# Performance work log

Measured on AMD Instinct MI355X. Metric: run time of the kernel, lower is better.

The kernel has to match this reference:

```python
import jax, jax.numpy as jnp
import numpy as np

N_NODES = 4096
N_EDGES = 65536
BS = 16
LEAKY_SLOPE = 0.01
BN_EPS = 1e-5


def _init(key, shape, scale=0.02):
    return (jax.random.normal(key, shape, dtype=jnp.float32) * scale)


def setup_inputs() -> dict:
    key = jax.random.key(0)
    ks = jax.random.split(key, 20)
    x_in = jax.random.normal(ks[0], (N_NODES, 8500), dtype=jnp.float32)
    edge_index = jax.random.randint(ks[1], (2, N_EDGES), 0, N_NODES, dtype=jnp.int64)
    return {
        "x_in": x_in,
        "edge_index": edge_index,
        # SAGEConv params: Wl (neighbor lin, with bias), Wr (root lin, no bias)
        "W1l": _init(ks[2], (320, 8500)), "b1": jnp.zeros((320,), jnp.float32), "W1r": _init(ks[3], (320, 8500)),
        "W2l": _init(ks[4], (180, 320)),  "b2": jnp.zeros((180,), jnp.float32), "W2r": _init(ks[5], (180, 320)),
        "W3l": _init(ks[6], (90, 180)),   "b3": jnp.zeros((90,), jnp.float32),  "W3r": _init(ks[7], (90, 180)),
        "W4l": _init(ks[8], (50, 90)),    "b4": jnp.zeros((50,), jnp.float32),  "W4r": _init(ks[9], (50, 90)),
        "Wf1": _init(ks[10], (32, 50)),   "bf1": jnp.zeros((32,), jnp.float32),
        "Wf2": _init(ks[11], (16, 32)),   "bf2": jnp.zeros((16,), jnp.float32),
        "Wf3": _init(ks[12], (1, 16)),    "bf3": jnp.zeros((1,), jnp.float32),
    }


def _sage(x, src, dst, Wl, bl, Wr):
    # PyG SAGEConv: out = lin_l(mean_{j in N(i)} x_j) + lin_r(x_i)
    agg = jax.ops.segment_sum(x[src], dst, num_segments=N_NODES)          # [N, F]
    deg = jax.ops.segment_sum(jnp.ones_like(dst, dtype=x.dtype), dst, num_segments=N_NODES)
    mean = agg / jnp.maximum(deg, 1.0)[:, None]
    return mean @ Wl.T + bl + x @ Wr.T


def _leaky(x):
    return jnp.where(x >= 0, x, LEAKY_SLOPE * x)


def _bn(x):
    # F.batch_norm(x, None, None, training=True): per-feature, biased var, no affine
    m = jnp.mean(x, axis=0)
    v = jnp.mean((x - m) ** 2, axis=0)
    return (x - m) / jnp.sqrt(v + BN_EPS)


def reference(x_in, edge_index,
              W1l, b1, W1r, W2l, b2, W2r, W3l, b3, W3r, W4l, b4, W4r,
              Wf1, bf1, Wf2, bf2, Wf3, bf3):
    src, dst = edge_index[0], edge_index[1]
    x = _bn(_leaky(_sage(x_in, src, dst, W1l, b1, W1r)))
    x = _bn(_leaky(_sage(x, src, dst, W2l, b2, W2r)))
    x = _bn(_leaky(_sage(x, src, dst, W3l, b3, W3r)))
    x = _bn(_leaky(_sage(x, src, dst, W4l, b4, W4r)))
    # get_batch: label i -> floor(i / (N/BS)); global_add_pool == segment sum
    x = x.reshape(BS, N_NODES // BS, -1).sum(axis=1)                      # [BS, 50]
    x = x @ Wf1.T + bf1
    x = x @ Wf2.T + bf2
    x = x @ Wf3.T + bf3
    return x
```

## Files before the change

### kernel.cpp

```cpp
#include <hip/hip_runtime.h>
#include <stdint.h>

#define NN 4096
#define NE 65536
#define LEAKY 0.01f
#define BN_EPS 1e-5f

typedef float f32x4 __attribute__((ext_vector_type(4)));
typedef __bf16 bf16x8 __attribute__((ext_vector_type(8)));

static __device__ __forceinline__ unsigned short f2bf(float v) {
  unsigned int u = __float_as_uint(v);
  u += 0x7fff + ((u >> 16) & 1);
  return (unsigned short)(u >> 16);
}

typedef __attribute__((address_space(1))) void gvoid;
typedef __attribute__((address_space(3))) void lvoid;

static __device__ __forceinline__ void async16(const void* g, void* l) {
  __builtin_amdgcn_global_load_lds((gvoid*)(uintptr_t)g,
                                   (lvoid*)(uint32_t)(uintptr_t)l, 16, 0, 0);
}


__global__ void pack_x1(const float* __restrict__ x, unsigned short* __restrict__ out) {
  int idx = blockIdx.x * 256 + threadIdx.x;
  int row = idx / 8512;
  int k = idx - row * 8512;
  float v = (k < 8500) ? x[(size_t)row * 8500 + k] : 0.f;
  out[idx] = f2bf(v);
}

__global__ void pack_w(const float* __restrict__ Wl, const float* __restrict__ Wr,
                       unsigned short* __restrict__ dst, int Fout, int Fin, int Kp, int total) {
  int idx = blockIdx.x * 256 + threadIdx.x;
  if (idx >= total) return;
  int row = idx / Kp;
  int k = idx - row * Kp;
  float v = 0.f;
  if (k < Fin) {
    if (row < Fout)            v = Wl[(size_t)row * Fin + k];
    else if (row < 2 * Fout)   v = Wr[(size_t)(row - Fout) * Fin + k];
  }
  dst[idx] = f2bf(v);
}


__global__ void count_deg(const int* __restrict__ dst_idx, int* __restrict__ deg) {
  int e = blockIdx.x * 256 + threadIdx.x;
  if (e < NE) atomicAdd(&deg[dst_idx[e]], 1);
}

__global__ __launch_bounds__(1024) void scan_deg(const int* __restrict__ deg,
                                                 int* __restrict__ off) {
  __shared__ int s[NN];
  int t = threadIdx.x;
  for (int i = t; i < NN; i += 1024) s[i] = deg[i];
  __syncthreads();
  for (int step = 1; step < NN; step <<= 1) {
    int v[4];
#pragma unroll
    for (int j = 0; j < 4; ++j) {
      int i = t + j * 1024;
      v[j] = (i >= step) ? s[i - step] : 0;
    }
    __syncthreads();
#pragma unroll
    for (int j = 0; j < 4; ++j) s[t + j * 1024] += v[j];
    __syncthreads();
  }
  for (int i = t; i < NN; i += 1024) off[i] = (i == 0) ? 0 : s[i - 1];
}

__global__ void scatter_edges(const int* __restrict__ src_idx,
                              const int* __restrict__ dst_idx,
                              const int* __restrict__ off, int* __restrict__ cursor,
                              int* __restrict__ eix) {
  int e = blockIdx.x * 256 + threadIdx.x;
  if (e < NE) {
    int d = dst_idx[e];
    int pos = atomicAdd(&cursor[d], 1);
    eix[off[d] + pos] = src_idx[e];
  }
}

__global__ __launch_bounds__(256) void gemm_bt(const unsigned short* __restrict__ A,
                                               const unsigned short* __restrict__ B,
                                               float* __restrict__ C, int N, int K) {
  __shared__ unsigned short smem[2 * 128 * 64];
  unsigned short* As = smem;
  unsigned short* Bs = smem + 128 * 64;

  const int t = threadIdx.x;
  const int bm = blockIdx.x, bn = blockIdx.y;
  const int lane = t & 63;
  const int wave = t >> 6;
  const int wm = (wave & 1) * 64, wn = (wave >> 1) * 64;
  const int l16 = lane & 15, quad = lane >> 4;

  const int ksteps = K >> 6;
  const int gz = (int)gridDim.z;
  const int per = (ksteps + gz - 1) / gz;
  const int k0 = (int)blockIdx.z * per;
  int k1 = k0 + per; if (k1 > ksteps) k1 = ksteps;

  f32x4 zero = {0.f, 0.f, 0.f, 0.f};
  f32x4 acc[4][4];
#pragma unroll
  for (int i = 0; i < 4; ++i)
#pragma unroll
    for (int j = 0; j < 4; ++j) acc[i][j] = zero;

  const int srow = t >> 3;
  const int scol = (t & 7) * 8;
  const unsigned short* Abase = A + (size_t)(bm * 128) * K + scol;
  const unsigned short* Bbase = B + (size_t)(bn * 128) * K + scol;

  for (int kt = k0; kt < k1; ++kt) {
    const unsigned short* Ag = Abase + kt * 64;
    const unsigned short* Bg = Bbase + kt * 64;
#pragma unroll
    for (int p = 0; p < 4; ++p) {
      int row = p * 32 + srow;
      async16(Ag + (size_t)row * K, &As[row * 64 + scol]);
    }
#pragma unroll
    for (int p = 0; p < 4; ++p) {
      int row = p * 32 + srow;
      async16(Bg + (size_t)row * K, &Bs[row * 64 + scol]);
    }
    __syncthreads();
#pragma unroll
    for (int kh = 0; kh < 2; ++kh) {
      bf16x8 af[4], bfr[4];
#pragma unroll
      for (int i = 0; i < 4; ++i)
        af[i] = *(const bf16x8*)&As[(wm + i * 16 + l16) * 64 + kh * 32 + quad * 8];
#pragma unroll
      for (int j = 0; j < 4; ++j)
        bfr[j] = *(const bf16x8*)&Bs[(wn + j * 16 + l16) * 64 + kh * 32 + quad * 8];
#pragma unroll
      for (int i = 0; i < 4; ++i)
#pragma unroll
        for (int j = 0; j < 4; ++j)
          acc[i][j] = __builtin_amdgcn_mfma_f32_16x16x32_bf16(af[i], bfr[j], acc[i][j], 0, 0, 0);
    }
    __syncthreads();
  }

  const bool use_atomic = (gridDim.z > 1);
#pragma unroll
  for (int i = 0; i < 4; ++i) {
    int rbase = bm * 128 + wm + i * 16 + quad * 4;
#pragma unroll
    for (int j = 0; j < 4; ++j) {
      int col = bn * 128 + wn + j * 16 + l16;
      float* cp = C + (size_t)rbase * N + col;
#pragma unroll
      for (int r = 0; r < 4; ++r) {
        if (use_atomic) atomicAdd(cp + (size_t)r * N, acc[i][j][r]);
        else            cp[(size_t)r * N] = acc[i][j][r];
      }
    }
  }
}

__global__ void sage_agg(const float* __restrict__ y, const int* __restrict__ off,
                         const int* __restrict__ deg, const int* __restrict__ eix,
                         const float* __restrict__ bias, float* __restrict__ z,
                         int F, int ldy) {
  int i = blockIdx.x;
  int f = blockIdx.y * 64 + threadIdx.x;
  if (f >= F) return;
  int start = off[i], d = deg[i];
  float s = 0.f;
  for (int e = 0; e < d; ++e) {
    int src = eix[start + e];
    s += y[(size_t)src * ldy + f];
  }
  int dm = d > 1 ? d : 1;
  float v = s / (float)dm + y[(size_t)i * ldy + F + f] + bias[f];
  z[(size_t)i * F + f] = (v >= 0.f) ? v : LEAKY * v;
}


__global__ void bn_stats(const float* __restrict__ z, float* __restrict__ mrs, int F) {
  int f = blockIdx.x;
  int t = threadIdx.x;
  float s = 0.f, s2 = 0.f;
  for (int i = t; i < NN; i += 256) {
    float v = z[(size_t)i * F + f];
    s += v; s2 += v * v;
  }
  __shared__ float rs[256], rs2[256];
  rs[t] = s; rs2[t] = s2;
  __syncthreads();
  for (int o = 128; o > 0; o >>= 1) {
    if (t < o) { rs[t] += rs[t + o]; rs2[t] += rs2[t + o]; }
    __syncthreads();
  }
  if (t == 0) {
    float m = rs[0] * (1.f / NN);
    float var = rs2[0] * (1.f / NN) - m * m;
    mrs[f] = m;
    mrs[F + f] = 1.f / sqrtf(var + BN_EPS);
  }
}

__global__ void bn_norm_bf16(const float* __restrict__ z, const float* __restrict__ mrs,
                             unsigned short* __restrict__ xout, int F, int Kp, int total) {
  int idx = blockIdx.x * 256 + threadIdx.x;
  if (idx >= total) return;
  int row = idx / Kp;
  int k = idx - row * Kp;
  float v = 0.f;
  if (k < F) v = (z[(size_t)row * F + k] - mrs[k]) * mrs[F + k];
  xout[idx] = f2bf(v);
}

__global__ void bn_norm_f32(const float* __restrict__ z, const float* __restrict__ mrs,
                            float* __restrict__ xout, int F, int total) {
  int idx = blockIdx.x * 256 + threadIdx.x;
  if (idx >= total) return;
  int row = idx / F;
  int k = idx - row * F;
  xout[idx] = (z[(size_t)row * F + k] - mrs[k]) * mrs[F + k];
}

__global__ void pool_fc(const float* __restrict__ x,
                        const float* __restrict__ Wf1, const float* __restrict__ bf1,
                        const float* __restrict__ Wf2, const float* __restrict__ bf2,
                        const float* __restrict__ Wf3, const float* __restrict__ bf3,
                        float* __restrict__ out) {
  __shared__ float pool[50];
  __shared__ float h1[32], h2[16];
  int b = blockIdx.x, t = threadIdx.x;
  if (t < 50) {
    float s = 0.f;
    for (int r = 0; r < 256; ++r) s += x[(size_t)(b * 256 + r) * 50 + t];
    pool[t] = s;
  }
  __syncthreads();
  if (t < 32) {
    float s = bf1[t];
    for (int f = 0; f < 50; ++f) s += pool[f] * Wf1[t * 50 + f];
    h1[t] = s;
  }
  __syncthreads();
  if (t < 16) {
    float s = bf2[t];
    for (int f = 0; f < 32; ++f) s += h1[f] * Wf2[t * 32 + f];
    h2[t] = s;
  }
  __syncthreads();
  if (t == 0) {
    float s = bf3[0];
    for (int f = 0; f < 16; ++f) s += h2[f] * Wf3[f];
    out[b] = s;
  }
}


extern "C" void kernel_launch(void* const* d_in, const int* in_sizes, int n_in,
                              void* d_out, int out_size, void* d_ws, size_t ws_size,
                              hipStream_t stream) {
  const float* x_in = (const float*)d_in[0];
  const int* ei = (const int*)d_in[1];
  const float* W1l = (const float*)d_in[2];
  const float* b1  = (const float*)d_in[3];
  const float* W1r = (const float*)d_in[4];
  const float* W2l = (const float*)d_in[5];
  const float* b2  = (const float*)d_in[6];
  const float* W2r = (const float*)d_in[7];
  const float* W3l = (const float*)d_in[8];
  const float* b3  = (const float*)d_in[9];
  const float* W3r = (const float*)d_in[10];
  const float* W4l = (const float*)d_in[11];
  const float* b4  = (const float*)d_in[12];
  const float* W4r = (const float*)d_in[13];
  const float* Wf1 = (const float*)d_in[14];
  const float* bf1 = (const float*)d_in[15];
  const float* Wf2 = (const float*)d_in[16];
  const float* bf2 = (const float*)d_in[17];
  const float* Wf3 = (const float*)d_in[18];
  const float* bf3 = (const float*)d_in[19];
  float* out = (float*)d_out;
  (void)in_sizes; (void)n_in; (void)out_size;

  char* ws = (char*)d_ws;
  size_t off = 0;
  auto alloc = [&](size_t bytes) -> void* {
    void* p = ws + off;
    off = (off + bytes + 255) & ~(size_t)255;
    return p;
  };
  unsigned short* xbf = (unsigned short*)alloc((size_t)NN * 8512 * 2);
  unsigned short* wb1 = (unsigned short*)alloc((size_t)640 * 8512 * 2);
  unsigned short* wb2 = (unsigned short*)alloc((size_t)384 * 320 * 2);
  unsigned short* wb3 = (unsigned short*)alloc((size_t)256 * 192 * 2);
  unsigned short* wb4 = (unsigned short*)alloc((size_t)128 * 128 * 2);
  float* y    = (float*)alloc((size_t)NN * 640 * 4);
  float* z    = (float*)alloc((size_t)NN * 320 * 4);
  float* z4   = (float*)alloc((size_t)NN * 50 * 4);
  float* mrs  = (float*)alloc(2 * 320 * 4);
  int* deg    = (int*)alloc(NN * 4);
  int* cursor = (int*)alloc(NN * 4);
  int* offb   = (int*)alloc(NN * 4);
  int* eix    = (int*)alloc(NE * 4);
  if (ws_size < off) return;

  hipMemsetAsync(deg, 0, 2 * NN * 4, stream);
  hipMemsetAsync(y, 0, (size_t)NN * 640 * 4, stream);

  pack_x1<<<dim3((NN * 8512) / 256), dim3(256), 0, stream>>>(x_in, xbf);
  pack_w<<<dim3((640 * 8512) / 256), dim3(256), 0, stream>>>(W1l, W1r, wb1, 320, 8500, 8512, 640 * 8512);
  pack_w<<<dim3((384 * 320 + 255) / 256), dim3(256), 0, stream>>>(W2l, W2r, wb2, 180, 320, 320, 384 * 320);
  pack_w<<<dim3((256 * 192 + 255) / 256), dim3(256), 0, stream>>>(W3l, W3r, wb3, 90, 180, 192, 256 * 192);
  pack_w<<<dim3((128 * 128 + 255) / 256), dim3(256), 0, stream>>>(W4l, W4r, wb4, 50, 90, 128, 128 * 128);
  count_deg<<<dim3(NE / 256), dim3(256), 0, stream>>>(ei + NE, deg);
  scan_deg<<<dim3(1), dim3(1024), 0, stream>>>(deg, offb);
  scatter_edges<<<dim3(NE / 256), dim3(256), 0, stream>>>(ei, ei + NE, offb, cursor, eix);

  gemm_bt<<<dim3(32, 5, 4), dim3(256), 0, stream>>>(xbf, wb1, y, 640, 8512);
  sage_agg<<<dim3(NN, 5), dim3(64), 0, stream>>>(y, offb, deg, eix, b1, z, 320, 640);
  bn_stats<<<dim3(320), dim3(256), 0, stream>>>(z, mrs, 320);
  bn_norm_bf16<<<dim3((NN * 320) / 256), dim3(256), 0, stream>>>(z, mrs, xbf, 320, 320, NN * 320);

  gemm_bt<<<dim3(32, 3, 1), dim3(256), 0, stream>>>(xbf, wb2, y, 384, 320);
  sage_agg<<<dim3(NN, 3), dim3(64), 0, stream>>>(y, offb, deg, eix, b2, z, 180, 384);
  bn_stats<<<dim3(180), dim3(256), 0, stream>>>(z, mrs, 180);
  bn_norm_bf16<<<dim3((NN * 192) / 256), dim3(256), 0, stream>>>(z, mrs, xbf, 180, 192, NN * 192);

  gemm_bt<<<dim3(32, 2, 1), dim3(256), 0, stream>>>(xbf, wb3, y, 256, 192);
  sage_agg<<<dim3(NN, 2), dim3(64), 0, stream>>>(y, offb, deg, eix, b3, z, 90, 256);
  bn_stats<<<dim3(90), dim3(256), 0, stream>>>(z, mrs, 90);
  bn_norm_bf16<<<dim3((NN * 128) / 256), dim3(256), 0, stream>>>(z, mrs, xbf, 90, 128, NN * 128);

  gemm_bt<<<dim3(32, 1, 1), dim3(256), 0, stream>>>(xbf, wb4, y, 128, 128);
  sage_agg<<<dim3(NN, 1), dim3(64), 0, stream>>>(y, offb, deg, eix, b4, z, 50, 128);
  bn_stats<<<dim3(50), dim3(256), 0, stream>>>(z, mrs, 50);
  bn_norm_f32<<<dim3((NN * 50) / 256), dim3(256), 0, stream>>>(z, mrs, z4, 50, NN * 50);

  pool_fc<<<dim3(16), dim3(64), 0, stream>>>(z4, Wf1, bf1, Wf2, bf2, Wf3, bf3, out);
}
```

Measured before the change: 569.4 us.

## Fuse setup kernels, swizzle LDS layout, split BN stats, fold last BN into pooling

Merges the x/weight bf16 packing and degree counting into one vectorized setup kernel that writes 8-element chunks in a row-rotated swizzled order. The GEMM reads LDS with the matching swizzle to cut bank conflicts. BN statistics become a parallel partial-sum kernel with atomics, and normalization is fused into a vectorized bf16 writer. The last BN is folded algebraically into the pooling kernel, and the layer-1 GEMM split-K rises from 4 to 8. The atomic float sums make results order-dependent, and the single-pass variance can lose precision.

```diff
diff --git a/kernel.cpp b/kernel.cpp
--- a/kernel.cpp
+++ b/kernel.cpp
@@ -8,6 +8,7 @@
 
 typedef float f32x4 __attribute__((ext_vector_type(4)));
 typedef __bf16 bf16x8 __attribute__((ext_vector_type(8)));
+typedef unsigned short u16x8 __attribute__((ext_vector_type(8)));
 
 static __device__ __forceinline__ unsigned short f2bf(float v) {
   unsigned int u = __float_as_uint(v);
@@ -24,33 +25,84 @@
 }
 
 
-__global__ void pack_x1(const float* __restrict__ x, unsigned short* __restrict__ out) {
-  int idx = blockIdx.x * 256 + threadIdx.x;
-  int row = idx / 8512;
-  int k = idx - row * 8512;
-  float v = (k < 8500) ? x[(size_t)row * 8500 + k] : 0.f;
-  out[idx] = f2bf(v);
-}
-
-__global__ void pack_w(const float* __restrict__ Wl, const float* __restrict__ Wr,
-                       unsigned short* __restrict__ dst, int Fout, int Fin, int Kp, int total) {
-  int idx = blockIdx.x * 256 + threadIdx.x;
-  if (idx >= total) return;
-  int row = idx / Kp;
-  int k = idx - row * Kp;
-  float v = 0.f;
-  if (k < Fin) {
-    if (row < Fout)            v = Wl[(size_t)row * Fin + k];
-    else if (row < 2 * Fout)   v = Wr[(size_t)(row - Fout) * Fin + k];
-  }
-  dst[idx] = f2bf(v);
-}
-
-
-__global__ void count_deg(const int* __restrict__ dst_idx, int* __restrict__ deg) {
-  int e = blockIdx.x * 256 + threadIdx.x;
-  if (e < NE) atomicAdd(&deg[dst_idx[e]], 1);
-}
+static __device__ __forceinline__ void pack_w_seg(int lblk, const float* __restrict__ Wl,
+                                                  const float* __restrict__ Wr,
+                                                  unsigned short* __restrict__ dst,
+                                                  int Fout, int Fin, int Kp, int Np) {
+  int nb = Kp >> 3;
+  int idx = lblk * 256 + threadIdx.x;
+  if (idx >= Np * nb) return;
+  int row = idx / nb, kb = idx - row * nb;
+  int g = kb >> 3, b = kb & 7;
+  int dkb = (g << 3) | ((b + row) & 7);
+  const float* src = nullptr;
+  if (row < Fout)          src = Wl + (size_t)row * Fin;
+  else if (row < 2 * Fout) src = Wr + (size_t)(row - Fout) * Fin;
+  u16x8 st;
+#pragma unroll
+  for (int o = 0; o < 8; ++o) {
+    int k = kb * 8 + o;
+    float v = (src && k < Fin) ? src[k] : 0.f;
+    st[o] = f2bf(v);
+  }
+  *(u16x8*)&dst[(size_t)row * Kp + dkb * 8] = st;
+}
+
+#define PX_BLK   17024
+#define PW1_BLK   2660
+#define PW2_BLK     60
+#define PW3_BLK     24
+#define PW4_BLK      8
+#define CD_BLK     256
+#define SETUP_BLK (PX_BLK + PW1_BLK + PW2_BLK + PW3_BLK + PW4_BLK + CD_BLK)
+
+__global__ __launch_bounds__(256) void setup_all(
+    const float* __restrict__ x, const int* __restrict__ dsti,
+    const float* __restrict__ W1l, const float* __restrict__ W1r,
+    const float* __restrict__ W2l, const float* __restrict__ W2r,
+    const float* __restrict__ W3l, const float* __restrict__ W3r,
+    const float* __restrict__ W4l, const float* __restrict__ W4r,
+    unsigned short* __restrict__ xbf, unsigned short* __restrict__ wb1,
+    unsigned short* __restrict__ wb2, unsigned short* __restrict__ wb3,
+    unsigned short* __restrict__ wb4, int* __restrict__ deg) {
+  int blk = blockIdx.x;
+  if (blk < PX_BLK) {
+    int idx = blk * 256 + threadIdx.x;
+    int row = idx / 1064, kb = idx - row * 1064;
+    int g = kb >> 3, b = kb & 7;
+    int dkb = (g << 3) | ((b + row) & 7);
+    const float* src = x + (size_t)row * 8500 + kb * 8;
+    float v[8];
+    if (kb < 1062) {
+      f32x4 a = *(const f32x4*)src;
+      f32x4 c = *(const f32x4*)(src + 4);
+#pragma unroll
+      for (int o = 0; o < 4; ++o) { v[o] = a[o]; v[o + 4] = c[o]; }
+    } else {
+#pragma unroll
+      for (int o = 0; o < 8; ++o) {
+        int k = kb * 8 + o;
+        v[o] = (k < 8500) ? x[(size_t)row * 8500 + k] : 0.f;
+      }
+    }
+    u16x8 st;
+#pragma unroll
+    for (int o = 0; o < 8; ++o) st[o] = f2bf(v[o]);
+    *(u16x8*)&xbf[(size_t)row * 8512 + dkb * 8] = st;
+  } else if (blk < PX_BLK + PW1_BLK) {
+    pack_w_seg(blk - PX_BLK, W1l, W1r, wb1, 320, 8500, 8512, 640);
+  } else if (blk < PX_BLK + PW1_BLK + PW2_BLK) {
+    pack_w_seg(blk - PX_BLK - PW1_BLK, W2l, W2r, wb2, 180, 320, 320, 384);
+  } else if (blk < PX_BLK + PW1_BLK + PW2_BLK + PW3_BLK) {
+    pack_w_seg(blk - PX_BLK - PW1_BLK - PW2_BLK, W3l, W3r, wb3, 90, 180, 192, 256);
+  } else if (blk < PX_BLK + PW1_BLK + PW2_BLK + PW3_BLK + PW4_BLK) {
+    pack_w_seg(blk - PX_BLK - PW1_BLK - PW2_BLK - PW3_BLK, W4l, W4r, wb4, 50, 90, 128, 128);
+  } else {
+    int e = (blk - (SETUP_BLK - CD_BLK)) * 256 + threadIdx.x;
+    atomicAdd(&deg[dsti[e]], 1);
+  }
+}
+
 
 __global__ __launch_bounds__(1024) void scan_deg(const int* __restrict__ deg,
                                                  int* __restrict__ off) {
@@ -133,13 +185,14 @@
     __syncthreads();
 #pragma unroll
     for (int kh = 0; kh < 2; ++kh) {
+      const int s8 = ((kh * 4 + quad + l16) & 7) * 8;
       bf16x8 af[4], bfr[4];
 #pragma unroll
       for (int i = 0; i < 4; ++i)
-        af[i] = *(const bf16x8*)&As[(wm + i * 16 + l16) * 64 + kh * 32 + quad * 8];
+        af[i] = *(const bf16x8*)&As[(wm + i * 16 + l16) * 64 + s8];
 #pragma unroll
       for (int j = 0; j < 4; ++j)
-        bfr[j] = *(const bf16x8*)&Bs[(wn + j * 16 + l16) * 64 + kh * 32 + quad * 8];
+        bfr[j] = *(const bf16x8*)&Bs[(wn + j * 16 + l16) * 64 + s8];
 #pragma unroll
       for (int i = 0; i < 4; ++i)
 #pragma unroll
@@ -185,50 +238,54 @@
 }
 
 
-__global__ void bn_stats(const float* __restrict__ z, float* __restrict__ mrs, int F) {
-  int f = blockIdx.x;
-  int t = threadIdx.x;
+__global__ __launch_bounds__(256) void bn_part(const float* __restrict__ z,
+                                               float* __restrict__ sums, int F) {
+  int tx = threadIdx.x, ty = threadIdx.y;
+  int f = blockIdx.x * 64 + tx;
   float s = 0.f, s2 = 0.f;
-  for (int i = t; i < NN; i += 256) {
-    float v = z[(size_t)i * F + f];
-    s += v; s2 += v * v;
-  }
-  __shared__ float rs[256], rs2[256];
-  rs[t] = s; rs2[t] = s2;
+  if (f < F) {
+    int r0 = blockIdx.y * 512 + ty * 128;
+    for (int j = 0; j < 128; ++j) {
+      float v = z[(size_t)(r0 + j) * F + f];
+      s += v; s2 += v * v;
+    }
+  }
+  __shared__ float ls[4][64], ls2[4][64];
+  ls[ty][tx] = s; ls2[ty][tx] = s2;
   __syncthreads();
-  for (int o = 128; o > 0; o >>= 1) {
-    if (t < o) { rs[t] += rs[t + o]; rs2[t] += rs2[t + o]; }
-    __syncthreads();
-  }
-  if (t == 0) {
-    float m = rs[0] * (1.f / NN);
-    float var = rs2[0] * (1.f / NN) - m * m;
-    mrs[f] = m;
-    mrs[F + f] = 1.f / sqrtf(var + BN_EPS);
-  }
-}
-
-__global__ void bn_norm_bf16(const float* __restrict__ z, const float* __restrict__ mrs,
-                             unsigned short* __restrict__ xout, int F, int Kp, int total) {
+  if (ty == 0 && f < F) {
+    float S  = ls[0][tx] + ls[1][tx] + ls[2][tx] + ls[3][tx];
+    float S2 = ls2[0][tx] + ls2[1][tx] + ls2[2][tx] + ls2[3][tx];
+    atomicAdd(&sums[f], S);
+    atomicAdd(&sums[F + f], S2);
+  }
+}
+
+__global__ void bn_norm8(const float* __restrict__ z, const float* __restrict__ sums,
+                         unsigned short* __restrict__ xout, int F, int Kp) {
+  int nb = Kp >> 3;
   int idx = blockIdx.x * 256 + threadIdx.x;
-  if (idx >= total) return;
-  int row = idx / Kp;
-  int k = idx - row * Kp;
-  float v = 0.f;
-  if (k < F) v = (z[(size_t)row * F + k] - mrs[k]) * mrs[F + k];
-  xout[idx] = f2bf(v);
-}
-
-__global__ void bn_norm_f32(const float* __restrict__ z, const float* __restrict__ mrs,
-                            float* __restrict__ xout, int F, int total) {
-  int idx = blockIdx.x * 256 + threadIdx.x;
-  if (idx >= total) return;
-  int row = idx / F;
-  int k = idx - row * F;
-  xout[idx] = (z[(size_t)row * F + k] - mrs[k]) * mrs[F + k];
-}
-
-__global__ void pool_fc(const float* __restrict__ x,
+  int row = idx / nb, kb = idx - row * nb;
+  int g = kb >> 3, b = kb & 7;
+  int dkb = (g << 3) | ((b + row) & 7);
+  u16x8 st;
+#pragma unroll
+  for (int o = 0; o < 8; ++o) {
+    int k = kb * 8 + o;
+    float v = 0.f;
+    if (k < F) {
+      float m  = sums[k] * (1.f / NN);
+      float var = sums[F + k] * (1.f / NN) - m * m;
+      float rs = rsqrtf(var + BN_EPS);
+      v = (z[(size_t)row * F + k] - m) * rs;
+    }
+    st[o] = f2bf(v);
+  }
+  *(u16x8*)&xout[(size_t)row * Kp + dkb * 8] = st;
+}
+
+__global__ void pool_fc(const float* __restrict__ z,
+                        const float* __restrict__ sums,
                         const float* __restrict__ Wf1, const float* __restrict__ bf1,
                         const float* __restrict__ Wf2, const float* __restrict__ bf2,
                         const float* __restrict__ Wf3, const float* __restrict__ bf3,
@@ -238,8 +295,11 @@
   int b = blockIdx.x, t = threadIdx.x;
   if (t < 50) {
     float s = 0.f;
-    for (int r = 0; r < 256; ++r) s += x[(size_t)(b * 256 + r) * 50 + t];
-    pool[t] = s;
+    for (int r = 0; r < 256; ++r) s += z[(size_t)(b * 256 + r) * 50 + t];
+    float m  = sums[t] * (1.f / NN);
+    float var = sums[50 + t] * (1.f / NN) - m * m;
+    float rs = rsqrtf(var + BN_EPS);
+    pool[t] = (s - 256.f * m) * rs;
   }
   __syncthreads();
   if (t < 32) {
@@ -302,45 +362,44 @@
   unsigned short* wb4 = (unsigned short*)alloc((size_t)128 * 128 * 2);
   float* y    = (float*)alloc((size_t)NN * 640 * 4);
   float* z    = (float*)alloc((size_t)NN * 320 * 4);
-  float* z4   = (float*)alloc((size_t)NN * 50 * 4);
-  float* mrs  = (float*)alloc(2 * 320 * 4);
   int* deg    = (int*)alloc(NN * 4);
   int* cursor = (int*)alloc(NN * 4);
+  float* bnsum = (float*)alloc(1280 * 4);
   int* offb   = (int*)alloc(NN * 4);
   int* eix    = (int*)alloc(NE * 4);
   if (ws_size < off) return;
-
-  hipMemsetAsync(deg, 0, 2 * NN * 4, stream);
+  float* bns1 = bnsum;
+  float* bns2 = bnsum + 640;
+  float* bns3 = bnsum + 1000;
+  float* bns4 = bnsum + 1180;
+
+  hipMemsetAsync(deg, 0, 2 * NN * 4 + 1280 * 4, stream);
   hipMemsetAsync(y, 0, (size_t)NN * 640 * 4, stream);
 
-  pack_x1<<<dim3((NN * 8512) / 256), dim3(256), 0, stream>>>(x_in, xbf);
-  pack_w<<<dim3((640 * 8512) / 256), dim3(256), 0, stream>>>(W1l, W1r, wb1, 320, 8500, 8512, 640 * 8512);
-  pack_w<<<dim3((384 * 320 + 255) / 256), dim3(256), 0, stream>>>(W2l, W2r, wb2, 180, 320, 320, 384 * 320);
-  pack_w<<<dim3((256 * 192 + 255) / 256), dim3(256), 0, stream>>>(W3l, W3r, wb3, 90, 180, 192, 256 * 192);
-  pack_w<<<dim3((128 * 128 + 255) / 256), dim3(256), 0, stream>>>(W4l, W4r, wb4, 50, 90, 128, 128 * 128);
-  count_deg<<<dim3(NE / 256), dim3(256), 0, stream>>>(ei + NE, deg);
+  setup_all<<<dim3(SETUP_BLK), dim3(256), 0, stream>>>(
+      x_in, ei + NE, W1l, W1r, W2l, W2r, W3l, W3r, W4l, W4r,
+      xbf, wb1, wb2, wb3, wb4, deg);
   scan_deg<<<dim3(1), dim3(1024), 0, stream>>>(deg, offb);
   scatter_edges<<<dim3(NE / 256), dim3(256), 0, stream>>>(ei, ei + NE, offb, cursor, eix);
 
-  gemm_bt<<<dim3(32, 5, 4), dim3(256), 0, stream>>>(xbf, wb1, y, 640, 8512);
+  gemm_bt<<<dim3(32, 5, 8), dim3(256), 0, stream>>>(xbf, wb1, y, 640, 8512);
   sage_agg<<<dim3(NN, 5), dim3(64), 0, stream>>>(y, offb, deg, eix, b1, z, 320, 640);
-  bn_stats<<<dim3(320), dim3(256), 0, stream>>>(z, mrs, 320);
-  bn_norm_bf16<<<dim3((NN * 320) / 256), dim3(256), 0, stream>>>(z, mrs, xbf, 320, 320, NN * 320);
+  bn_part<<<dim3(5, 8), dim3(64, 4), 0, stream>>>(z, bns1, 320);
+  bn_norm8<<<dim3(NN * 40 / 256), dim3(256), 0, stream>>>(z, bns1, xbf, 320, 320);
 
   gemm_bt<<<dim3(32, 3, 1), dim3(256), 0, stream>>>(xbf, wb2, y, 384, 320);
   sage_agg<<<dim3(NN, 3), dim3(64), 0, stream>>>(y, offb, deg, eix, b2, z, 180, 384);
-  bn_stats<<<dim3(180), dim3(256), 0, stream>>>(z, mrs, 180);
-  bn_norm_bf16<<<dim3((NN * 192) / 256), dim3(256), 0, stream>>>(z, mrs, xbf, 180, 192, NN * 192);
+  bn_part<<<dim3(3, 8), dim3(64, 4), 0, stream>>>(z, bns2, 180);
+  bn_norm8<<<dim3(NN * 24 / 256), dim3(256), 0, stream>>>(z, bns2, xbf, 180, 192);
 
   gemm_bt<<<dim3(32, 2, 1), dim3(256), 0, stream>>>(xbf, wb3, y, 256, 192);
   sage_agg<<<dim3(NN, 2), dim3(64), 0, stream>>>(y, offb, deg, eix, b3, z, 90, 256);
-  bn_stats<<<dim3(90), dim3(256), 0, stream>>>(z, mrs, 90);
-  bn_norm_bf16<<<dim3((NN * 128) / 256), dim3(256), 0, stream>>>(z, mrs, xbf, 90, 128, NN * 128);
+  bn_part<<<dim3(2, 8), dim3(64, 4), 0, stream>>>(z, bns3, 90);
+  bn_norm8<<<dim3(NN * 16 / 256), dim3(256), 0, stream>>>(z, bns3, xbf, 90, 128);
 
   gemm_bt<<<dim3(32, 1, 1), dim3(256), 0, stream>>>(xbf, wb4, y, 128, 128);
   sage_agg<<<dim3(NN, 1), dim3(64), 0, stream>>>(y, offb, deg, eix, b4, z, 50, 128);
-  bn_stats<<<dim3(50), dim3(256), 0, stream>>>(z, mrs, 50);
-  bn_norm_f32<<<dim3((NN * 50) / 256), dim3(256), 0, stream>>>(z, mrs, z4, 50, NN * 50);
-
-  pool_fc<<<dim3(16), dim3(64), 0, stream>>>(z4, Wf1, bf1, Wf2, bf2, Wf3, bf3, out);
-}
+  bn_part<<<dim3(1, 8), dim3(64, 4), 0, stream>>>(z, bns4, 50);
+
+  pool_fc<<<dim3(16), dim3(64), 0, stream>>>(z, bns4, Wf1, bf1, Wf2, bf2, Wf3, bf3, out);
+}
```

Result: no change. 559.5 us (-1.7%).
